# Performance work log

Hardware: AMD Instinct MI355X
Metric: run time of the kernel (lower is better)

Reference implementation:

```python
import jax, jax.numpy as jnp
import numpy as np

DIM = 256
EXP = 4
EPS_DYT = 1e-5
EPS_ATTN = 1e-5
TEMP = 10000.0


def _linear(x, w, b):
    # torch nn.Linear: y = x @ W^T + b, W is [out, in]
    return jnp.einsum('...i,oi->...o', x, w) + b


def _dwconv3x3(x_nhwc, w, b):
    # depthwise 3x3, padding=1; w: [C,1,3,3]
    xc = x_nhwc.transpose(0, 3, 1, 2)
    y = jax.lax.conv_general_dilated(
        xc, w, window_strides=(1, 1), padding='SAME',
        feature_group_count=w.shape[0],
        dimension_numbers=('NCHW', 'OIHW', 'NCHW'))
    return y.transpose(0, 2, 3, 1) + b


def _dyt(x, gamma, beta):
    mu = x.mean(axis=-1, keepdims=True)
    sd = x.std(axis=-1, keepdims=True, ddof=1) + EPS_DYT  # torch std is unbiased
    return jnp.tanh(gamma * (x - mu) / sd + beta)


def _mona(x, w, b):
    # SE-style: global avg pool -> fc -> sigmoid -> channel gate
    s = jax.nn.sigmoid(_linear(x.mean(axis=(1, 2)), w, b))  # [B,C]
    return x * s[:, None, None, :]


def _pos_emb(H, W, C):
    dq = C // 4
    omega = 1.0 / (TEMP ** (jnp.arange(dq, dtype=jnp.float32) / dq))
    xo = jnp.arange(W, dtype=jnp.float32)[:, None] * omega  # [W,dq]
    yo = jnp.arange(H, dtype=jnp.float32)[:, None] * omega  # [H,dq]
    xe = jnp.concatenate([jnp.sin(xo), jnp.cos(xo)], axis=-1)  # [W,2dq]
    ye = jnp.concatenate([jnp.sin(yo), jnp.cos(yo)], axis=-1)  # [H,2dq]
    pos = jnp.concatenate([
        jnp.broadcast_to(xe[None, :, :], (H, W, 2 * dq)),
        jnp.broadcast_to(ye[:, None, :], (H, W, 2 * dq))], axis=-1)  # [H,W,C]
    return pos


def setup_inputs() -> dict:
    key = jax.random.key(0)
    ks = jax.random.split(key, 16)
    d = DIM
    dh = d * EXP
    w = lambda k, shape: jax.random.normal(k, shape, dtype=jnp.float32) * 0.02
    return {
        'x': jax.random.normal(ks[0], (8, d // 4, 64, 64), dtype=jnp.float32),
        'in_proj_w': w(ks[1], (d, d // 4)),
        'wq_w': w(ks[2], (d, d)), 'wq_b': jnp.zeros((d,), jnp.float32),
        'wk_w': w(ks[3], (d, d)), 'wk_b': jnp.zeros((d,), jnp.float32),
        'wv_w': w(ks[4], (d, d)), 'wv_b': jnp.zeros((d,), jnp.float32),
        'wo_w': w(ks[5], (d, d)), 'wo_b': jnp.zeros((d,), jnp.float32),
        'psi_w': w(ks[6], (d, 1, 3, 3)), 'psi_b': jnp.zeros((d,), jnp.float32),
        'dyt_g': jnp.ones((d,), jnp.float32), 'dyt_b': jnp.zeros((d,), jnp.float32),
        'm1_w': w(ks[7], (d, d)), 'm1_b': jnp.zeros((d,), jnp.float32),
        'm2_w': w(ks[8], (d, d)), 'm2_b': jnp.zeros((d,), jnp.float32),
        'we_w': w(ks[9], (dh, d)), 'we_b': jnp.zeros((dh,), jnp.float32),
        'dw_w': w(ks[10], (dh, 1, 3, 3)), 'dw_b': jnp.zeros((dh,), jnp.float32),
        'wp_w': w(ks[11], (d, dh)), 'wp_b': jnp.zeros((d,), jnp.float32),
        'out_proj_w': w(ks[12], (d // 4, d)),
    }


def _sapa(x, wq_w, wq_b, wk_w, wk_b, wv_w, wv_b, wo_w, wo_b, psi_w, psi_b):
    B, H, W, C = x.shape
    N = H * W
    pos = _pos_emb(H, W, C).reshape(N, C)
    psi = jax.nn.sigmoid(_dwconv3x3(x, psi_w, psi_b)).reshape(B, N, C)
    xf = x.reshape(B, N, C)
    Q = psi * (_linear(xf, wq_w, wq_b) + pos)
    K = psi * (_linear(xf, wk_w, wk_b) + pos)
    V = _linear(xf, wv_w, wv_b)
    phi_Q = jnp.square(jax.nn.relu(Q))
    phi_K = jnp.square(jax.nn.relu(K))
    # attn / (phiQ @ sum_n phiK + eps) @ V  ==  (phiQ @ (phiK^T V)) / (phiQ @ ksum + eps)
    kv = jnp.einsum('bnc,bnd->bcd', phi_K, V)           # [B,C,C]
    num = jnp.einsum('bnc,bcd->bnd', phi_Q, kv)         # [B,N,C]
    den = jnp.einsum('bnc,bc->bn', phi_Q, phi_K.sum(axis=1))[..., None] + EPS_ATTN
    out = _linear(num / den, wo_w, wo_b)
    return out.reshape(B, H, W, C)


def _edffn(x, we_w, we_b, dw_w, dw_b, wp_w, wp_b):
    h = _linear(x, we_w, we_b)                 # [B,H,W,4C]
    h = jax.nn.gelu(_dwconv3x3(h, dw_w, dw_b))
    return x + _linear(h, wp_w, wp_b)


def reference(x, in_proj_w, wq_w, wq_b, wk_w, wk_b, wv_w, wv_b, wo_w, wo_b,
              psi_w, psi_b, dyt_g, dyt_b, m1_w, m1_b, m2_w, m2_b,
              we_w, we_b, dw_w, dw_b, wp_w, wp_b, out_proj_w):
    # in_proj: 1x1 conv (no bias; eval-BN is identity) + SiLU -> NHWC
    h = jax.nn.silu(jnp.einsum('bchw,oc->bhwo', x, in_proj_w))
    a = _sapa(h, wq_w, wq_b, wk_w, wk_b, wv_w, wv_b, wo_w, wo_b, psi_w, psi_b)
    U1 = _mona(_dyt(h + a, dyt_g, dyt_b), m1_w, m1_b)
    U2 = U1 + _edffn(U1, we_w, we_b, dw_w, dw_b, wp_w, wp_b)
    Y = _mona(_dyt(U2, dyt_g, dyt_b), m2_w, m2_b)
    return jax.nn.silu(jnp.einsum('bhwc,oc->bohw', Y, out_proj_w))
```

## Files before the change

kernel.cpp:

```cpp
#include <hip/hip_runtime.h>
#include <hip/hip_bf16.h>
#include <cmath>

using bf16 = __hip_bfloat16;
using bf16x8 = __attribute__((ext_vector_type(8))) short;
using bf16x4 = __attribute__((ext_vector_type(4))) short;
using f32x4v = __attribute__((ext_vector_type(4))) float;

static constexpr int BB  = 8;
static constexpr int HW  = 64;
static constexpr int NN  = HW * HW;
static constexpr int CC  = 256;
static constexpr int CIN = 64;
static constexpr int DH  = 1024;
static constexpr int MM  = BB * NN;

__device__ __forceinline__ bf16 f2b(float v) { return __float2bfloat16(v); }
__device__ __forceinline__ float b2f(bf16 v) { return __bfloat162float(v); }
__device__ __forceinline__ float tf(float v) { return v; }
__device__ __forceinline__ float tf(bf16 v)  { return b2f(v); }
__device__ __forceinline__ float frcp(float x) { return __builtin_amdgcn_rcpf(x); }
__device__ __forceinline__ float sigmf(float x) { return frcp(1.f + __expf(-x)); }
__device__ __forceinline__ float siluf(float x) { return x * sigmf(x); }
__device__ __forceinline__ float geluf(float x) {
  float z = x * fmaf(x * x, 0.07135481627f, 1.5957691216f);
  return x * sigmf(z);
}
__device__ __forceinline__ float tanhfast(float x) {
  return 1.f - 2.f * frcp(1.f + __expf(2.f * x));
}

__device__ __forceinline__ void stage16(const bf16* g, bf16* l) {
  __builtin_amdgcn_global_load_lds(
      (const __attribute__((address_space(1))) void*)g,
      (__attribute__((address_space(3))) void*)l, 16, 0, 0);
}

__global__ __launch_bounds__(256) void pos_kern(float* __restrict__ pos) {
  int n = blockIdx.x, o = threadIdx.x;
  int yy = n >> 6, xx = n & 63;
  int i = o & 63, q = o >> 6;
  float omega = __expf((float)i * -0.14391156831212787f);
  float coord = (q < 2) ? (float)xx : (float)yy;
  float ang = coord * omega;
  pos[(size_t)n * CC + o] = (q & 1) ? __cosf(ang) : __sinf(ang);
}

__global__ __launch_bounds__(256) void cvt_weights(
    const float* __restrict__ wq, const float* __restrict__ wk,
    const float* __restrict__ wv, const float* __restrict__ wo,
    const float* __restrict__ we, const float* __restrict__ wp,
    const float* __restrict__ qb, const float* __restrict__ kb,
    const float* __restrict__ vb,
    bf16* __restrict__ wqkvb, bf16* __restrict__ wob,
    bf16* __restrict__ web, bf16* __restrict__ wpb,
    float* __restrict__ bqkv, float* __restrict__ ksum) {
  int i = blockIdx.x * 256 + threadIdx.x;
  switch (blockIdx.y) {
    case 0: if (i < 65536) wqkvb[i] = f2b(wq[i]);
            if (i < 2048) ksum[i] = 0.f;
            break;
    case 1: if (i < 65536) wqkvb[65536 + i] = f2b(wk[i]);
            if (i < 768) bqkv[i] = (i < 256) ? qb[i] : (i < 512) ? kb[i - 256] : vb[i - 512];
            break;
    case 2: if (i < 65536) wqkvb[131072 + i] = f2b(wv[i]); break;
    case 3: if (i < 65536) wob[i] = f2b(wo[i]); break;
    case 4: web[i] = f2b(we[i]); break;
    case 5: wpb[i] = f2b(wp[i]); break;
  }
}

__global__ __launch_bounds__(256) void inproj_tile(const float* __restrict__ X,
                                                   const float* __restrict__ W,
                                                   float* __restrict__ H,
                                                   bf16* __restrict__ Hb) {
  __shared__ float Xs[16][68];
  __shared__ float Ws[16][68];
  int m0 = blockIdx.x * 64, o0 = blockIdx.y * 64, b = blockIdx.z;
  int tid = threadIdx.x, tx = tid & 15, ty = tid >> 4;
  float acc[4][4] = {};
  for (int k0 = 0; k0 < CIN; k0 += 16) {
    {
      int mm = tid & 63, kk0 = tid >> 6;
#pragma unroll
      for (int i = 0; i < 4; ++i) {
        int kk = kk0 * 4 + i;
        Xs[kk][mm] = X[((size_t)(b * CIN + k0 + kk)) * NN + m0 + mm];
      }
    }
    {
      int kk = tid & 15, oo0 = tid >> 4;
#pragma unroll
      for (int i = 0; i < 4; ++i) {
        int oo = oo0 + i * 16;
        Ws[kk][oo] = W[(size_t)(o0 + oo) * CIN + k0 + kk];
      }
    }
    __syncthreads();
#pragma unroll
    for (int kk = 0; kk < 16; ++kk) {
      float xv[4], wv[4];
#pragma unroll
      for (int a = 0; a < 4; ++a) xv[a] = Xs[kk][ty * 4 + a];
#pragma unroll
      for (int c = 0; c < 4; ++c) wv[c] = Ws[kk][tx * 4 + c];
#pragma unroll
      for (int a = 0; a < 4; ++a)
#pragma unroll
        for (int c = 0; c < 4; ++c) acc[a][c] += xv[a] * wv[c];
    }
    __syncthreads();
  }
#pragma unroll
  for (int a = 0; a < 4; ++a) {
    int m = m0 + ty * 4 + a;
#pragma unroll
    for (int c = 0; c < 4; ++c) {
      int o = o0 + tx * 4 + c;
      float v = siluf(acc[a][c]);
      size_t idx = ((size_t)b * NN + m) * CC + o;
      H[idx] = v;
      Hb[idx] = f2b(v);
    }
  }
}

__global__ __launch_bounds__(256) void outproj_tile(const float* __restrict__ T2,
                                                    const float* __restrict__ gate,
                                                    const float* __restrict__ W,
                                                    float* __restrict__ Y) {
  __shared__ float Xs[16][68];
  __shared__ float Ws[16][68];
  int n0 = blockIdx.x * 64, b = blockIdx.z;
  size_t mbase = (size_t)b * NN;
  const float* gb = gate + b * CC;
  int tid = threadIdx.x, tx = tid & 15, ty = tid >> 4;
  float acc[4][4] = {};
  for (int k0 = 0; k0 < CC; k0 += 16) {
    int kk = tid & 15, rr0 = tid >> 4;
    float gk = gb[k0 + kk];
#pragma unroll
    for (int i = 0; i < 4; ++i) {
      int rr = rr0 + i * 16;
      Xs[kk][rr] = T2[(mbase + n0 + rr) * CC + k0 + kk] * gk;
      Ws[kk][rr] = (rr < CIN) ? W[(size_t)rr * CC + k0 + kk] : 0.f;
    }
    __syncthreads();
#pragma unroll
    for (int kk2 = 0; kk2 < 16; ++kk2) {
      float xv[4], wv[4];
#pragma unroll
      for (int a = 0; a < 4; ++a) xv[a] = Xs[kk2][ty * 4 + a];
#pragma unroll
      for (int c = 0; c < 4; ++c) wv[c] = Ws[kk2][tx * 4 + c];
#pragma unroll
      for (int a = 0; a < 4; ++a)
#pragma unroll
        for (int c = 0; c < 4; ++c) acc[a][c] += xv[a] * wv[c];
    }
    __syncthreads();
  }
#pragma unroll
  for (int a = 0; a < 4; ++a) {
    int n = n0 + ty * 4 + a;
#pragma unroll
    for (int c = 0; c < 4; ++c) {
      int o = tx * 4 + c;
      if (o < CIN)
        Y[(size_t)(b * CIN + o) * NN + n] = siluf(acc[a][c]);
    }
  }
}

enum { EPI_PLAIN = 0, EPI_BIAS = 1, EPI_NUM = 3, EPI_RESID = 4, EPI_ADD1 = 5 };

__device__ __forceinline__ void storeO(float* p, float v) { *p = v; }
__device__ __forceinline__ void storeO(bf16* p, float v) { *p = f2b(v); }

template <int EPI, bool WPB, bool KVS, bool XSWZ, bool BM64, typename YT, typename A2T>
__global__ __launch_bounds__(256) void gemm_bf16(const bf16* __restrict__ X,
                                                 const bf16* __restrict__ W,
                                                 const float* __restrict__ bias,
                                                 YT* __restrict__ Y, int Kd, int Od,
                                                 const float* __restrict__ aux1,
                                                 const A2T* __restrict__ aux2) {
  constexpr int BM  = BM64 ? 64 : 128;
  constexpr int NNT = BM64 ? 2 : 4;
  __shared__ __align__(16) bf16 As[BM * 32];
  __shared__ __align__(16) bf16 Bs[128 * 32];
  int m0, o0;
  if (XSWZ) {
    int gy = gridDim.y;
    int nwg = gridDim.x * gy;
    int lin = blockIdx.y * gridDim.x + blockIdx.x;
    int q = nwg >> 3;
    int lin2 = (lin & 7) * q + (lin >> 3);
    m0 = (lin2 / gy) * BM;
    o0 = (lin2 % gy) * 128;
  } else {
    m0 = blockIdx.x * BM;
    o0 = blockIdx.y * 128;
  }
  int kbeg = 0, kend = Kd;
  if (KVS) {
    int b = blockIdx.z >> 4, ks = blockIdx.z & 15;
    size_t off = (size_t)b * CC * Kd;
    X += off; W += off;
    Y += (size_t)blockIdx.z * CC * CC;
    kbeg = ks * (Kd / 16); kend = kbeg + Kd / 16;
  }
  const bf16* Wp = WPB ? (W + (size_t)(m0 >> 12) * Kd * Od) : W;
  int t = threadIdx.x;
  int l = t & 63, w = t >> 6;
  int wm = BM64 ? 0 : (w >> 1) * 64;
  int wn = BM64 ? w * 32 : (w & 1) * 64;
  int lr = l & 15, lq = l >> 4;
  int srow = t >> 2, skc = (t & 3) * 8;
  f32x4v acc[4][NNT] = {};
  for (int k0 = kbeg; k0 < kend; k0 += 32) {
    stage16(X + (size_t)(m0 + srow) * Kd + k0 + skc, As + t * 8);
    if (!BM64)
      stage16(X + (size_t)(m0 + 64 + srow) * Kd + k0 + skc, As + 2048 + t * 8);
    stage16(Wp + (size_t)(o0 + srow) * Kd + k0 + skc, Bs + t * 8);
    stage16(Wp + (size_t)(o0 + 64 + srow) * Kd + k0 + skc, Bs + 2048 + t * 8);
    __syncthreads();
    bf16x8 af[4], bfr[NNT];
#pragma unroll
    for (int mt = 0; mt < 4; ++mt)
      af[mt] = *(const bf16x8*)(As + (wm + mt * 16 + lr) * 32 + lq * 8);
#pragma unroll
    for (int nt = 0; nt < NNT; ++nt)
      bfr[nt] = *(const bf16x8*)(Bs + (wn + nt * 16 + lr) * 32 + lq * 8);
#pragma unroll
    for (int mt = 0; mt < 4; ++mt)
#pragma unroll
      for (int nt = 0; nt < NNT; ++nt)
        acc[mt][nt] = __builtin_amdgcn_mfma_f32_16x16x32_bf16(af[mt], bfr[nt], acc[mt][nt], 0, 0, 0);
    __syncthreads();
  }
#pragma unroll
  for (int nt = 0; nt < NNT; ++nt) {
    int o = o0 + wn + nt * 16 + lr;
    float bv = (EPI == EPI_PLAIN || EPI == EPI_NUM) ? 0.f : bias[o];
#pragma unroll
    for (int mt = 0; mt < 4; ++mt) {
      int mb = m0 + wm + mt * 16 + lq * 4;
#pragma unroll
      for (int r = 0; r < 4; ++r) {
        int m = mb + r;
        float v = acc[mt][nt][r] + bv;
        if constexpr (EPI == EPI_PLAIN || EPI == EPI_BIAS) {
          storeO(Y + (size_t)m * Od + o, v);
        } else if constexpr (EPI == EPI_NUM) {
          storeO(Y + (size_t)m * Od + o, v * aux1[m]);
        } else if constexpr (EPI == EPI_ADD1) {
          storeO(Y + (size_t)m * Od + o, v + tf(aux2[(size_t)m * Od + o]));
        } else {
          int gb = m >> 12;
          float u1 = tf(aux2[(size_t)m * Od + o]) * aux1[gb * CC + o];
          storeO(Y + (size_t)m * Od + o, v + 2.f * u1);
        }
      }
    }
  }
}

__global__ __launch_bounds__(256) void qkmath_kern(const bf16* __restrict__ QKV,
                                                   const float* __restrict__ pose,
                                                   const bf16* __restrict__ psi,
                                                   bf16* __restrict__ PQ,
                                                   bf16* __restrict__ KT,
                                                   bf16* __restrict__ VTo,
                                                   float* __restrict__ ksum) {
  __shared__ bf16 Ts[64][258];
  int sec = blockIdx.y;
  int m0 = blockIdx.x * 64;
  int b = m0 >> 12, n0 = m0 & (NN - 1);
  int t = threadIdx.x;
  int cg = (t & 31) * 8;
  int rg = t >> 5;
  if (sec == 0) {
#pragma unroll
    for (int p = 0; p < 8; ++p) {
      int r = p * 8 + rg;
      size_t m = (size_t)m0 + r;
      int n = (int)(m & (NN - 1));
      union { bf16x8 v; bf16 e[8]; } qv, pv, ov;
      qv.v = *(const bf16x8*)(QKV + m * 768 + cg);
      pv.v = *(const bf16x8*)(psi + m * CC + cg);
      const float* pr = pose + (size_t)n * CC + cg;
      f32x4v p0 = *(const f32x4v*)pr;
      f32x4v p1 = *(const f32x4v*)(pr + 4);
#pragma unroll
      for (int j = 0; j < 8; ++j) {
        float pj = (j < 4) ? p0[j] : p1[j - 4];
        float v = (b2f(qv.e[j]) + pj) * b2f(pv.e[j]);
        v = fmaxf(v, 0.f);
        ov.e[j] = f2b(v * v);
      }
      *(bf16x8*)(PQ + m * CC + cg) = ov.v;
    }
    return;
  }
  const bool KM = (sec == 1);
#pragma unroll
  for (int p = 0; p < 8; ++p) {
    int r = p * 8 + rg;
    size_t m = (size_t)m0 + r;
    union { bf16x8 v; bf16 e[8]; } qv, ov;
    qv.v = *(const bf16x8*)(QKV + m * 768 + sec * 256 + cg);
    if (KM) {
      int n = (int)(m & (NN - 1));
      union { bf16x8 v; bf16 e[8]; } pv;
      pv.v = *(const bf16x8*)(psi + m * CC + cg);
      const float* pr = pose + (size_t)n * CC + cg;
      f32x4v p0 = *(const f32x4v*)pr;
      f32x4v p1 = *(const f32x4v*)(pr + 4);
#pragma unroll
      for (int j = 0; j < 8; ++j) {
        float pj = (j < 4) ? p0[j] : p1[j - 4];
        float v = (b2f(qv.e[j]) + pj) * b2f(pv.e[j]);
        v = fmaxf(v, 0.f);
        ov.e[j] = f2b(v * v);
      }
    } else {
      ov.v = qv.v;
    }
    *(bf16x8*)(&Ts[r][cg]) = ov.v;
  }
  __syncthreads();
  int wv = t >> 6, lane = t & 63;
  bf16* base = KM ? KT : VTo;
  int nloc = (lane & 7) * 8;
  int gsub = lane >> 3;
#pragma unroll
  for (int k = 0; k < 8; ++k) {
    int c = wv * 64 + k * 8 + gsub;
    union { bf16x8 v; bf16 e[8]; } pk;
#pragma unroll
    for (int i = 0; i < 8; ++i) pk.e[i] = Ts[nloc + i][c];
    *(bf16x8*)(base + ((size_t)(b * CC + c)) * NN + n0 + nloc) = pk.v;
    if (KM) {
      float s = 0.f;
#pragma unroll
      for (int i = 0; i < 8; ++i) s += b2f(pk.e[i]);
      s += __shfl_xor(s, 1);
      s += __shfl_xor(s, 2);
      s += __shfl_xor(s, 4);
      if ((lane & 7) == 0) atomicAdd(&ksum[b * CC + c], s);
    }
  }
}

__global__ __launch_bounds__(256) void kvred_kern(const bf16* __restrict__ part,
                                                  bf16* __restrict__ kvTb) {
  int d = blockIdx.x, b = blockIdx.y, c = threadIdx.x;
  float s = 0.f;
#pragma unroll
  for (int ks = 0; ks < 16; ++ks)
    s += b2f(part[((size_t)(b * 16 + ks) * CC + d) * CC + c]);
  kvTb[((size_t)b * CC + d) * CC + c] = f2b(s);
}

__global__ __launch_bounds__(256) void den_kern(const bf16* __restrict__ PQ,
                                                const float* __restrict__ ksum,
                                                float* __restrict__ rden) {
  int b = blockIdx.y;
  int n = blockIdx.x * 4 + (threadIdx.x >> 6);
  int lane = threadIdx.x & 63;
  size_t m = (size_t)b * NN + n;
  union { bf16x4 v; bf16 e[4]; } u;
  u.v = *(const bf16x4*)(PQ + m * CC + lane * 4);
  const float* ks = ksum + b * CC + lane * 4;
  float s = 0.f;
#pragma unroll
  for (int j = 0; j < 4; ++j) s += b2f(u.e[j]) * ks[j];
#pragma unroll
  for (int off = 32; off >= 1; off >>= 1) s += __shfl_down(s, off);
  if (lane == 0) rden[m] = 1.f / (s + 1e-5f);
}

template <bool RESID>
__global__ __launch_bounds__(256) void dyt_kern(const float* __restrict__ X,
                                                const float* __restrict__ R,
                                                const float* __restrict__ g,
                                                const float* __restrict__ bt,
                                                float* __restrict__ T,
                                                float* __restrict__ poolq) {
  int wv = threadIdx.x >> 6;
  int m = blockIdx.x * 4 + wv;
  int lane = threadIdx.x & 63;
  size_t base = (size_t)m * CC + lane * 4;
  f32x4v x = *(const f32x4v*)(X + base);
  if constexpr (RESID) {
    f32x4v r = *(const f32x4v*)(R + base);
#pragma unroll
    for (int j = 0; j < 4; ++j) x[j] += r[j];
  }
  float s = (x[0] + x[1]) + (x[2] + x[3]);
  float q = fmaf(x[0], x[0], fmaf(x[1], x[1], fmaf(x[2], x[2], x[3] * x[3])));
#pragma unroll
  for (int off = 32; off >= 1; off >>= 1) {
    s += __shfl_xor(s, off);
    q += __shfl_xor(q, off);
  }
  float mu = s * (1.f / 256.f);
  float var = (q - 256.f * mu * mu) * (1.f / 255.f);
  float sd = sqrtf(fmaxf(var, 0.f)) + 1e-5f;
  float rs = frcp(sd);
  f32x4v gv = *(const f32x4v*)(g + lane * 4);
  f32x4v bv = *(const f32x4v*)(bt + lane * 4);
  f32x4v o;
#pragma unroll
  for (int j = 0; j < 4; ++j)
    o[j] = tanhfast(fmaf(gv[j] * (x[j] - mu), rs, bv[j]));
  *(f32x4v*)(T + base) = o;
  __shared__ float ps[4][260];
#pragma unroll
  for (int j = 0; j < 4; ++j) ps[wv][lane * 4 + j] = o[j];
  __syncthreads();
  if (wv == 0) {
    f32x4v pv;
#pragma unroll
    for (int j = 0; j < 4; ++j) {
      int c = lane * 4 + j;
      pv[j] = (ps[0][c] + ps[1][c]) + (ps[2][c] + ps[3][c]);
    }
    *(f32x4v*)(poolq + (size_t)blockIdx.x * 256 + lane * 4) = pv;
  }
}

__global__ __launch_bounds__(256) void poolred_kern(const float* __restrict__ poolq,
                                                    float* __restrict__ pool16) {
  int s = blockIdx.x, b = blockIdx.y, c = threadIdx.x;
  float acc = 0.f;
#pragma unroll 8
  for (int k = 0; k < 64; ++k)
    acc += poolq[((size_t)(b * 1024 + s * 64 + k)) * 256 + c];
  pool16[(size_t)(b * 16 + s) * 256 + c] = acc;
}

__global__ __launch_bounds__(256) void gate_kern(const float* __restrict__ pool16,
                                                 const float* __restrict__ w,
                                                 const float* __restrict__ bias,
                                                 float* __restrict__ gate) {
  int b = blockIdx.x, o = threadIdx.x;
  __shared__ float p[CC];
  float s = 0.f;
#pragma unroll
  for (int k = 0; k < 16; ++k) s += pool16[(size_t)(b * 16 + k) * 256 + o];
  p[o] = s * (1.f / 4096.f);
  __syncthreads();
  float acc = bias[o];
  for (int c = 0; c < CC; ++c) acc += p[c] * w[o * CC + c];
  gate[b * CC + o] = sigmf(acc);
}

__global__ __launch_bounds__(256) void scale_b16(const float* __restrict__ T,
                                                 const float* __restrict__ gate,
                                                 bf16* __restrict__ Ob) {
  size_t i4 = ((size_t)blockIdx.x * 256 + threadIdx.x) * 4;
  int b = (int)(i4 >> 20);
  int c = (int)(i4 & (CC - 1));
  f32x4v t = *(const f32x4v*)(T + i4);
  f32x4v gv = *(const f32x4v*)(gate + b * CC + c);
  union { bf16x4 v; bf16 e[4]; } ob;
#pragma unroll
  for (int j = 0; j < 4; ++j) ob.e[j] = f2b(t[j] * gv[j]);
  *(bf16x4*)(Ob + i4) = ob.v;
}

template <int STRIDE>
__device__ __forceinline__ void dw_loadrow_b16(float (&row)[3][4], const bf16* __restrict__ Xb,
                                               int yy, int x, int dl, int dr) {
  if (yy < 0 || yy >= HW) {
#pragma unroll
    for (int cx = 0; cx < 3; ++cx)
#pragma unroll
      for (int j = 0; j < 4; ++j) row[cx][j] = 0.f;
    return;
  }
  const bf16* base = Xb + ((size_t)yy * HW + x) * (size_t)STRIDE;
  union U { bf16x4 v; bf16 e[4]; } um, ul, ur;
  um.v = *(const bf16x4*)base;
  ul.v = *(const bf16x4*)(base + dl);
  ur.v = *(const bf16x4*)(base + dr);
#pragma unroll
  for (int j = 0; j < 4; ++j) {
    row[0][j] = b2f(ul.e[j]);
    row[1][j] = b2f(um.e[j]);
    row[2][j] = b2f(ur.e[j]);
  }
}

__global__ __launch_bounds__(256) void dwconv_psi_v2(const bf16* __restrict__ X,
                                                     const float* __restrict__ w,
                                                     const float* __restrict__ bias,
                                                     bf16* __restrict__ Y) {
  int i = blockIdx.x;
  int lin = (i & 7) * 64 + (i >> 3);
  int xg = lin & 15, yc = (lin >> 4) & 3, b = lin >> 6;
  int c0 = (threadIdx.x & 63) * 4;
  int x  = xg * 4 + (threadIdx.x >> 6);
  int y0 = yc * 16;
  const bf16* Xb = X + (size_t)b * NN * CC + c0;
  bf16* Yb      = Y + (size_t)b * NN * CC + c0;
  float wt[9][4], bs[4];
#pragma unroll
  for (int j = 0; j < 4; ++j) {
    bs[j] = bias[c0 + j];
#pragma unroll
    for (int t9 = 0; t9 < 9; ++t9) wt[t9][j] = w[(c0 + j) * 9 + t9];
  }
  const bool xl = (x > 0), xr = (x < HW - 1);
  if (!xl) {
#pragma unroll
    for (int j = 0; j < 4; ++j) wt[0][j] = wt[3][j] = wt[6][j] = 0.f;
  }
  if (!xr) {
#pragma unroll
    for (int j = 0; j < 4; ++j) wt[2][j] = wt[5][j] = wt[8][j] = 0.f;
  }
  const int dl = xl ? -CC : 0, dr = xr ? CC : 0;
  float win[5][3][4];
  dw_loadrow_b16<CC>(win[0], Xb, y0 - 1, x, dl, dr);
  dw_loadrow_b16<CC>(win[1], Xb, y0,     x, dl, dr);
  dw_loadrow_b16<CC>(win[2], Xb, y0 + 1, x, dl, dr);
  dw_loadrow_b16<CC>(win[3], Xb, y0 + 2, x, dl, dr);
#pragma unroll
  for (int ii = 0; ii < 16; ++ii) {
    dw_loadrow_b16<CC>(win[(ii + 4) % 5], Xb, y0 + ii + 3, x, dl, dr);
    const int rt = ii % 5, rm = (ii + 1) % 5, rb = (ii + 2) % 5;
    union { bf16x4 v; bf16 e[4]; } o;
#pragma unroll
    for (int j = 0; j < 4; ++j) {
      float a = bs[j];
#pragma unroll
      for (int cx = 0; cx < 3; ++cx) {
        a = fmaf(win[rt][cx][j], wt[cx][j], a);
        a = fmaf(win[rm][cx][j], wt[3 + cx][j], a);
        a = fmaf(win[rb][cx][j], wt[6 + cx][j], a);
      }
      o.e[j] = f2b(sigmf(a));
    }
    *(bf16x4*)(Yb + ((size_t)(y0 + ii) * HW + x) * (size_t)CC) = o.v;
  }
}

__global__ __launch_bounds__(256) void dwconv1024_v2(const bf16* __restrict__ X,
                                                     const float* __restrict__ w,
                                                     const float* __restrict__ bias,
                                                     bf16* __restrict__ Y) {
  int i = blockIdx.x;
  int lin = (i & 7) * 256 + (i >> 3);
  int x = lin & 63, yc = (lin >> 6) & 3, b = lin >> 8;
  int c0 = threadIdx.x * 4;
  int y0 = yc * 16;
  const bf16* Xb = X + (size_t)b * NN * DH + c0;
  bf16* Yb       = Y + (size_t)b * NN * DH + c0;
  float wt[9][4], bs[4];
#pragma unroll
  for (int j = 0; j < 4; ++j) {
    bs[j] = bias[c0 + j];
#pragma unroll
    for (int t9 = 0; t9 < 9; ++t9) wt[t9][j] = w[(c0 + j) * 9 + t9];
  }
  const bool xl = (x > 0), xr = (x < HW - 1);
  if (!xl) {
#pragma unroll
    for (int j = 0; j < 4; ++j) wt[0][j] = wt[3][j] = wt[6][j] = 0.f;
  }
  if (!xr) {
#pragma unroll
    for (int j = 0; j < 4; ++j) wt[2][j] = wt[5][j] = wt[8][j] = 0.f;
  }
  const int dl = xl ? -DH : 0, dr = xr ? DH : 0;
  float win[5][3][4];
  dw_loadrow_b16<DH>(win[0], Xb, y0 - 1, x, dl, dr);
  dw_loadrow_b16<DH>(win[1], Xb, y0,     x, dl, dr);
  dw_loadrow_b16<DH>(win[2], Xb, y0 + 1, x, dl, dr);
  dw_loadrow_b16<DH>(win[3], Xb, y0 + 2, x, dl, dr);
#pragma unroll
  for (int ii = 0; ii < 16; ++ii) {
    dw_loadrow_b16<DH>(win[(ii + 4) % 5], Xb, y0 + ii + 3, x, dl, dr);
    const int rt = ii % 5, rm = (ii + 1) % 5, rb = (ii + 2) % 5;
    union { bf16x4 v; bf16 e[4]; } o;
#pragma unroll
    for (int j = 0; j < 4; ++j) {
      float a = bs[j];
#pragma unroll
      for (int cx = 0; cx < 3; ++cx) {
        a = fmaf(win[rt][cx][j], wt[cx][j], a);
        a = fmaf(win[rm][cx][j], wt[3 + cx][j], a);
        a = fmaf(win[rb][cx][j], wt[6 + cx][j], a);
      }
      o.e[j] = f2b(geluf(a));
    }
    *(bf16x4*)(Yb + ((size_t)(y0 + ii) * HW + x) * (size_t)DH) = o.v;
  }
}

extern "C" void kernel_launch(void* const* d_in, const int* in_sizes, int n_in,
                              void* d_out, int out_size, void* d_ws, size_t ws_size,
                              hipStream_t stream) {
  (void)in_sizes; (void)n_in; (void)out_size; (void)ws_size;
  const float* x       = (const float*)d_in[0];
  const float* in_proj = (const float*)d_in[1];
  const float* wq_w = (const float*)d_in[2];   const float* wq_b = (const float*)d_in[3];
  const float* wk_w = (const float*)d_in[4];   const float* wk_b = (const float*)d_in[5];
  const float* wv_w = (const float*)d_in[6];   const float* wv_b = (const float*)d_in[7];
  const float* wo_w = (const float*)d_in[8];   const float* wo_b = (const float*)d_in[9];
  const float* psi_w = (const float*)d_in[10]; const float* psi_b = (const float*)d_in[11];
  const float* dyt_g = (const float*)d_in[12]; const float* dyt_b = (const float*)d_in[13];
  const float* m1_w = (const float*)d_in[14];  const float* m1_b = (const float*)d_in[15];
  const float* m2_w = (const float*)d_in[16];  const float* m2_b = (const float*)d_in[17];
  const float* we_w = (const float*)d_in[18];  const float* we_b = (const float*)d_in[19];
  const float* dw_w = (const float*)d_in[20];  const float* dw_b = (const float*)d_in[21];
  const float* wp_w = (const float*)d_in[22];  const float* wp_b = (const float*)d_in[23];
  const float* wout = (const float*)d_in[24];
  float* out = (float*)d_out;

  char* ws = (char*)d_ws;
  const size_t MB = 1u << 20;
  float* H     = (float*)(ws);
  float* T1    = (float*)(ws);
  float* A     = (float*)(ws + 32 * MB);
  bf16*  psiB  = (bf16*)(ws + 64 * MB);
  bf16*  numb  = (bf16*)(ws + 80 * MB);
  bf16*  phiQ  = (bf16*)(ws + 96 * MB);
  bf16*  Hb    = (bf16*)(ws + 112 * MB);
  bf16*  phiKT = (bf16*)(ws + 128 * MB);
  bf16*  VT    = (bf16*)(ws + 144 * MB);
  bf16*  QKVr  = (bf16*)(ws + 160 * MB);
  bf16*  kvpartB = (bf16*)(ws + 160 * MB);
  bf16*  e1    = (bf16*)(ws + 64 * MB);
  bf16*  e2    = (bf16*)(ws + 128 * MB);
  float* T2    = (float*)(ws + 64 * MB);
  bf16*  U1b   = (bf16*)(ws + 192 * MB);
  bf16* wqkvb = (bf16*)(ws + 208 * MB);
  bf16* wob   = wqkvb + 196608;
  bf16* web   = wob + 65536;
  bf16* wpb   = web + 262144;
  float* bqkv = (float*)(wpb + 262144);
  float* pose = (float*)(ws + 210 * MB);
  char*  small = ws + 214 * MB;
  float* ksum  = (float*)(small);
  float* rden  = (float*)(small + 64 * 1024);
  float* pool16 = (float*)(small + 192 * 1024);
  float* gate1 = (float*)(small + 704 * 1024);
  float* gate2 = (float*)(small + 720 * 1024);
  bf16*  kvTb  = (bf16*)(small + 768 * 1024);
  float* poolq = (float*)(ws + 216 * MB);

  dim3 blk(256);

  pos_kern<<<dim3(NN), blk, 0, stream>>>(pose);
  cvt_weights<<<dim3(1024, 6), blk, 0, stream>>>(wq_w, wk_w, wv_w, wo_w, we_w, wp_w,
                                                 wq_b, wk_b, wv_b,
                                                 wqkvb, wob, web, wpb, bqkv, ksum);
  inproj_tile<<<dim3(64, 4, BB), blk, 0, stream>>>(x, in_proj, H, Hb);

  dwconv_psi_v2<<<dim3(512), blk, 0, stream>>>(Hb, psi_w, psi_b, psiB);
  gemm_bf16<EPI_BIAS, false, false, true, false, bf16, float>
      <<<dim3(256, 6), blk, 0, stream>>>(Hb, wqkvb, bqkv, QKVr, CC, 768, nullptr, nullptr);
  qkmath_kern<<<dim3(MM / 64, 3), blk, 0, stream>>>(QKVr, pose, psiB, phiQ, phiKT, VT, ksum);
  gemm_bf16<EPI_PLAIN, false, true, false, false, bf16, float>
      <<<dim3(2, 2, 128), blk, 0, stream>>>(VT, phiKT, nullptr, kvpartB, NN, CC, nullptr, nullptr);
  kvred_kern<<<dim3(CC, BB), blk, 0, stream>>>(kvpartB, kvTb);
  den_kern<<<dim3(1024, BB), blk, 0, stream>>>(phiQ, ksum, rden);
  gemm_bf16<EPI_NUM, true, false, true, true, bf16, float>
      <<<dim3(512, 2), blk, 0, stream>>>(phiQ, kvTb, nullptr, numb, CC, CC, rden, nullptr);
  gemm_bf16<EPI_ADD1, false, false, true, true, float, float>
      <<<dim3(512, 2), blk, 0, stream>>>(numb, wob, wo_b, A, CC, CC, nullptr, H);

  dyt_kern<false><<<dim3(MM / 4), blk, 0, stream>>>(A, nullptr, dyt_g, dyt_b, T1, poolq);
  poolred_kern<<<dim3(16, BB), blk, 0, stream>>>(poolq, pool16);
  gate_kern<<<dim3(BB), blk, 0, stream>>>(pool16, m1_w, m1_b, gate1);
  scale_b16<<<dim3(MM / 4), blk, 0, stream>>>(T1, gate1, U1b);

  gemm_bf16<EPI_BIAS, false, false, true, false, bf16, float>
      <<<dim3(256, 8), blk, 0, stream>>>(U1b, web, we_b, e1, CC, DH, nullptr, nullptr);
  dwconv1024_v2<<<dim3(2048), blk, 0, stream>>>(e1, dw_w, dw_b, e2);
  gemm_bf16<EPI_RESID, false, false, true, true, float, float>
      <<<dim3(512, 2), blk, 0, stream>>>(e2, wpb, wp_b, A, DH, CC, gate1, T1);

  dyt_kern<false><<<dim3(MM / 4), blk, 0, stream>>>(A, nullptr, dyt_g, dyt_b, T2, poolq);
  poolred_kern<<<dim3(16, BB), blk, 0, stream>>>(poolq, pool16);
  gate_kern<<<dim3(BB), blk, 0, stream>>>(pool16, m2_w, m2_b, gate2);

  outproj_tile<<<dim3(64, 1, BB), blk, 0, stream>>>(T2, gate2, wout, out);
}
```

Before: 448.7 us.

## Drop 64-row GEMM tile variant and read gated bf16 U1 in residual epilogue

Removes the BM64 template path so every GEMM uses 128x128 tiles, halving the grid for the N=256 output GEMMs and increasing operand reuse per block. The EDFFN projection epilogue now adds the already-gated bf16 U1 buffer instead of recomputing T1 times gate1 from fp32 T1, which cuts epilogue traffic. The trade-off is fewer blocks for the small GEMMs (512 workgroups) and bf16 rounding of the residual term.

```diff
diff --git a/kernel.cpp b/kernel.cpp
--- a/kernel.cpp
+++ b/kernel.cpp
@@ -177,16 +177,14 @@
 __device__ __forceinline__ void storeO(float* p, float v) { *p = v; }
 __device__ __forceinline__ void storeO(bf16* p, float v) { *p = f2b(v); }
 
-template <int EPI, bool WPB, bool KVS, bool XSWZ, bool BM64, typename YT, typename A2T>
+template <int EPI, bool WPB, bool KVS, bool XSWZ, typename YT, typename A2T>
 __global__ __launch_bounds__(256) void gemm_bf16(const bf16* __restrict__ X,
                                                  const bf16* __restrict__ W,
                                                  const float* __restrict__ bias,
                                                  YT* __restrict__ Y, int Kd, int Od,
                                                  const float* __restrict__ aux1,
                                                  const A2T* __restrict__ aux2) {
-  constexpr int BM  = BM64 ? 64 : 128;
-  constexpr int NNT = BM64 ? 2 : 4;
-  __shared__ __align__(16) bf16 As[BM * 32];
+  __shared__ __align__(16) bf16 As[128 * 32];
   __shared__ __align__(16) bf16 Bs[128 * 32];
   int m0, o0;
   if (XSWZ) {
@@ -195,10 +193,10 @@
     int lin = blockIdx.y * gridDim.x + blockIdx.x;
     int q = nwg >> 3;
     int lin2 = (lin & 7) * q + (lin >> 3);
-    m0 = (lin2 / gy) * BM;
+    m0 = (lin2 / gy) * 128;
     o0 = (lin2 % gy) * 128;
   } else {
-    m0 = blockIdx.x * BM;
+    m0 = blockIdx.x * 128;
     o0 = blockIdx.y * 128;
   }
   int kbeg = 0, kend = Kd;
@@ -212,34 +210,32 @@
   const bf16* Wp = WPB ? (W + (size_t)(m0 >> 12) * Kd * Od) : W;
   int t = threadIdx.x;
   int l = t & 63, w = t >> 6;
-  int wm = BM64 ? 0 : (w >> 1) * 64;
-  int wn = BM64 ? w * 32 : (w & 1) * 64;
+  int wm = (w >> 1) * 64, wn = (w & 1) * 64;
   int lr = l & 15, lq = l >> 4;
   int srow = t >> 2, skc = (t & 3) * 8;
-  f32x4v acc[4][NNT] = {};
+  f32x4v acc[4][4] = {};
   for (int k0 = kbeg; k0 < kend; k0 += 32) {
     stage16(X + (size_t)(m0 + srow) * Kd + k0 + skc, As + t * 8);
-    if (!BM64)
-      stage16(X + (size_t)(m0 + 64 + srow) * Kd + k0 + skc, As + 2048 + t * 8);
+    stage16(X + (size_t)(m0 + 64 + srow) * Kd + k0 + skc, As + 2048 + t * 8);
     stage16(Wp + (size_t)(o0 + srow) * Kd + k0 + skc, Bs + t * 8);
     stage16(Wp + (size_t)(o0 + 64 + srow) * Kd + k0 + skc, Bs + 2048 + t * 8);
     __syncthreads();
-    bf16x8 af[4], bfr[NNT];
+    bf16x8 af[4], bfr[4];
 #pragma unroll
     for (int mt = 0; mt < 4; ++mt)
       af[mt] = *(const bf16x8*)(As + (wm + mt * 16 + lr) * 32 + lq * 8);
 #pragma unroll
-    for (int nt = 0; nt < NNT; ++nt)
+    for (int nt = 0; nt < 4; ++nt)
       bfr[nt] = *(const bf16x8*)(Bs + (wn + nt * 16 + lr) * 32 + lq * 8);
 #pragma unroll
     for (int mt = 0; mt < 4; ++mt)
 #pragma unroll
-      for (int nt = 0; nt < NNT; ++nt)
+      for (int nt = 0; nt < 4; ++nt)
         acc[mt][nt] = __builtin_amdgcn_mfma_f32_16x16x32_bf16(af[mt], bfr[nt], acc[mt][nt], 0, 0, 0);
     __syncthreads();
   }
 #pragma unroll
-  for (int nt = 0; nt < NNT; ++nt) {
+  for (int nt = 0; nt < 4; ++nt) {
     int o = o0 + wn + nt * 16 + lr;
     float bv = (EPI == EPI_PLAIN || EPI == EPI_NUM) ? 0.f : bias[o];
 #pragma unroll
@@ -256,9 +252,7 @@
         } else if constexpr (EPI == EPI_ADD1) {
           storeO(Y + (size_t)m * Od + o, v + tf(aux2[(size_t)m * Od + o]));
         } else {
-          int gb = m >> 12;
-          float u1 = tf(aux2[(size_t)m * Od + o]) * aux1[gb * CC + o];
-          storeO(Y + (size_t)m * Od + o, v + 2.f * u1);
+          storeO(Y + (size_t)m * Od + o, v + 2.f * tf(aux2[(size_t)m * Od + o]));
         }
       }
     }
@@ -661,28 +655,28 @@
   inproj_tile<<<dim3(64, 4, BB), blk, 0, stream>>>(x, in_proj, H, Hb);
 
   dwconv_psi_v2<<<dim3(512), blk, 0, stream>>>(Hb, psi_w, psi_b, psiB);
-  gemm_bf16<EPI_BIAS, false, false, true, false, bf16, float>
+  gemm_bf16<EPI_BIAS, false, false, true, bf16, float>
       <<<dim3(256, 6), blk, 0, stream>>>(Hb, wqkvb, bqkv, QKVr, CC, 768, nullptr, nullptr);
   qkmath_kern<<<dim3(MM / 64, 3), blk, 0, stream>>>(QKVr, pose, psiB, phiQ, phiKT, VT, ksum);
-  gemm_bf16<EPI_PLAIN, false, true, false, false, bf16, float>
+  gemm_bf16<EPI_PLAIN, false, true, false, bf16, float>
       <<<dim3(2, 2, 128), blk, 0, stream>>>(VT, phiKT, nullptr, kvpartB, NN, CC, nullptr, nullptr);
   kvred_kern<<<dim3(CC, BB), blk, 0, stream>>>(kvpartB, kvTb);
   den_kern<<<dim3(1024, BB), blk, 0, stream>>>(phiQ, ksum, rden);
-  gemm_bf16<EPI_NUM, true, false, true, true, bf16, float>
-      <<<dim3(512, 2), blk, 0, stream>>>(phiQ, kvTb, nullptr, numb, CC, CC, rden, nullptr);
-  gemm_bf16<EPI_ADD1, false, false, true, true, float, float>
-      <<<dim3(512, 2), blk, 0, stream>>>(numb, wob, wo_b, A, CC, CC, nullptr, H);
+  gemm_bf16<EPI_NUM, true, false, true, bf16, float>
+      <<<dim3(256, 2), blk, 0, stream>>>(phiQ, kvTb, nullptr, numb, CC, CC, rden, nullptr);
+  gemm_bf16<EPI_ADD1, false, false, true, float, float>
+      <<<dim3(256, 2), blk, 0, stream>>>(numb, wob, wo_b, A, CC, CC, nullptr, H);
 
   dyt_kern<false><<<dim3(MM / 4), blk, 0, stream>>>(A, nullptr, dyt_g, dyt_b, T1, poolq);
   poolred_kern<<<dim3(16, BB), blk, 0, stream>>>(poolq, pool16);
   gate_kern<<<dim3(BB), blk, 0, stream>>>(pool16, m1_w, m1_b, gate1);
   scale_b16<<<dim3(MM / 4), blk, 0, stream>>>(T1, gate1, U1b);
 
-  gemm_bf16<EPI_BIAS, false, false, true, false, bf16, float>
+  gemm_bf16<EPI_BIAS, false, false, true, bf16, float>
       <<<dim3(256, 8), blk, 0, stream>>>(U1b, web, we_b, e1, CC, DH, nullptr, nullptr);
   dwconv1024_v2<<<dim3(2048), blk, 0, stream>>>(e1, dw_w, dw_b, e2);
-  gemm_bf16<EPI_RESID, false, false, true, true, float, float>
-      <<<dim3(512, 2), blk, 0, stream>>>(e2, wpb, wp_b, A, DH, CC, gate1, T1);
+  gemm_bf16<EPI_RESID, false, false, true, float, bf16>
+      <<<dim3(256, 2), blk, 0, stream>>>(e2, wpb, wp_b, A, DH, CC, nullptr, U1b);
 
   dyt_kern<false><<<dim3(MM / 4), blk, 0, stream>>>(A, nullptr, dyt_g, dyt_b, T2, poolq);
   poolred_kern<<<dim3(16, BB), blk, 0, stream>>>(poolq, pool16);
```

Measured after the change: 445.4 us. About the same (-0.7%).
